# Performance work log

Measured on AMD Instinct MI355X. Metric: run time of the kernel, lower is better.

Reference implementation:

```python
import jax, jax.numpy as jnp
import numpy as np

B, S, D, H = 2, 2048, 2048, 16
DH = D // H


def setup_inputs() -> dict:
    key = jax.random.key(0)
    k1, k2, k3 = jax.random.split(key, 3)
    x = jax.random.normal(k1, (B, S, D), dtype=jnp.float32)
    Wqkv = jax.random.normal(k2, (D, 3 * D), dtype=jnp.float32) * (1.0 / np.sqrt(D))
    bqkv = jnp.zeros((3 * D,), dtype=jnp.float32)
    Wproj = jax.random.normal(k3, (D, D), dtype=jnp.float32) * (1.0 / np.sqrt(D))
    bproj = jnp.zeros((D,), dtype=jnp.float32)
    return {"x": x, "Wqkv": Wqkv, "bqkv": bqkv, "Wproj": Wproj, "bproj": bproj}


def reference(x, Wqkv, bqkv, Wproj, bproj):
    b, s, d = x.shape
    h, dh = H, DH
    # fused qkv projection: [b, s, 3, h, dh]
    qkv = (x @ Wqkv + bqkv).reshape(b, s, 3, h, dh)
    q, k, v = qkv[:, :, 0], qkv[:, :, 1], qkv[:, :, 2]  # each [b, s, h, dh]
    scale = 1.0 / np.sqrt(dh).astype(np.float32)
    # scores [b, h, q, k]
    attn = jnp.einsum('bqhd,bkhd->bhqk', q, k) * scale
    causal = jnp.tril(jnp.ones((s, s), dtype=bool))  # [s, s]
    attn = jnp.where(causal[None, None], attn, -jnp.inf)
    attn = jax.nn.softmax(attn, axis=-1)
    out = jnp.einsum('bhqk,bkhd->bqhd', attn, v).reshape(b, s, d)
    return out @ Wproj + bproj
```

## Files before the change

### kernel.cpp

```cpp
#include <hip/hip_runtime.h>
#include <hip/hip_bf16.h>

#define BB 2
#define SS 2048
#define DD 2048
#define HH 16
#define DHH 128
#define MM 4096
#define NN1 6144
#define NTILES (DD / 64)

typedef __attribute__((ext_vector_type(8))) short bf16x8;
typedef __attribute__((ext_vector_type(4))) float f32x4;
typedef unsigned int u32;

static __device__ __forceinline__ float exp2_hw(float x) {
  return __builtin_amdgcn_exp2f(x);
}

static __device__ __forceinline__ unsigned short f2bf(float f) {
  union { float f; u32 u; } v; v.f = f;
  return (unsigned short)((v.u + 0x7FFFu + ((v.u >> 16) & 1u)) >> 16);
}

static __device__ __forceinline__ void gload_lds16(const void* g, void* l) {
  __builtin_amdgcn_global_load_lds((const __attribute__((address_space(1))) u32*)g,
                                   (__attribute__((address_space(3))) u32*)l, 16, 0, 0);
}

__global__ __launch_bounds__(256) void k_cvt(const float* __restrict__ in,
                                             unsigned short* __restrict__ out) {
  int i = blockIdx.x * 256 + threadIdx.x;
  float4 v = ((const float4*)in)[i];
  ushort4 o;
  o.x = f2bf(v.x); o.y = f2bf(v.y); o.z = f2bf(v.z); o.w = f2bf(v.w);
  ((ushort4*)out)[i] = o;
}

__global__ __launch_bounds__(256) void k_transpose(const float* __restrict__ in,
                                                   unsigned short* __restrict__ out,
                                                   int R, int C) {
  __shared__ float t[32][33];
  int bx = blockIdx.x * 32, by = blockIdx.y * 32;
  int tx = threadIdx.x, ty = threadIdx.y;
  #pragma unroll
  for (int i = ty; i < 32; i += 8)
    t[i][tx] = in[(size_t)(by + i) * C + bx + tx];
  __syncthreads();
  #pragma unroll
  for (int i = ty; i < 32; i += 8)
    out[(size_t)(bx + i) * R + by + tx] = f2bf(t[tx][i]);
}

__device__ __forceinline__ void gemm_core192(const char* __restrict__ Ag,
                                             const char* __restrict__ Bg,
                                             char* lds, f32x4 acc[8][3]) {
  const int tid = threadIdx.x;
  const int wave = tid >> 6, lane = tid & 63;
  const int g = lane >> 4, c = lane & 15;
  const int wm = wave >> 2, wn = wave & 3;

  auto stage = [&](int buf, int kt) {
    char* base = lds + buf * 57344;
    #pragma unroll
    for (int q = 0; q < 4; ++q) {
      int off = q * 8192 + tid * 16;
      int row = off >> 7, cb = off & 127;
      gload_lds16(Ag + (size_t)row * 4096 + kt * 128 + (cb ^ ((row & 7) << 4)),
                  base + q * 8192 + wave * 1024);
    }
    #pragma unroll
    for (int q = 0; q < 3; ++q) {
      int off = q * 8192 + tid * 16;
      int row = off >> 7, cb = off & 127;
      gload_lds16(Bg + (size_t)row * 4096 + kt * 128 + (cb ^ ((row & 7) << 4)),
                  base + 32768 + q * 8192 + wave * 1024);
    }
  };

  stage(0, 0);
  asm volatile("s_waitcnt vmcnt(0)" ::: "memory");
  __builtin_amdgcn_sched_barrier(0);
  __builtin_amdgcn_s_barrier();

  for (int t = 0; t < NTILES; ++t) {
    const char* Ab = lds + (t & 1) * 57344;
    const char* Bb = Ab + 32768;
    bf16x8 af[8][2], bfv[3][2];
    #pragma unroll
    for (int i = 0; i < 8; ++i) {
      int row = wm * 128 + i * 16 + c;
      af[i][0] = *(const bf16x8*)(Ab + row * 128 + ((g * 16) ^ ((row & 7) << 4)));
    }
    #pragma unroll
    for (int j = 0; j < 3; ++j) {
      int row = wn * 48 + j * 16 + c;
      bfv[j][0] = *(const bf16x8*)(Bb + row * 128 + ((g * 16) ^ ((row & 7) << 4)));
    }
    __builtin_amdgcn_sched_barrier(0);
    #pragma unroll
    for (int i = 0; i < 8; ++i) {
      int row = wm * 128 + i * 16 + c;
      af[i][1] = *(const bf16x8*)(Ab + row * 128 + ((64 + g * 16) ^ ((row & 7) << 4)));
    }
    #pragma unroll
    for (int j = 0; j < 3; ++j) {
      int row = wn * 48 + j * 16 + c;
      bfv[j][1] = *(const bf16x8*)(Bb + row * 128 + ((64 + g * 16) ^ ((row & 7) << 4)));
    }
    if (t + 1 < NTILES) stage((t + 1) & 1, t + 1);
    asm volatile("s_waitcnt lgkmcnt(11)" ::: "memory");
    __builtin_amdgcn_sched_barrier(0);
    __builtin_amdgcn_s_setprio(1);
    #pragma unroll
    for (int i = 0; i < 8; ++i)
      #pragma unroll
      for (int j = 0; j < 3; ++j)
        acc[i][j] = __builtin_amdgcn_mfma_f32_16x16x32_bf16(af[i][0], bfv[j][0], acc[i][j], 0, 0, 0);
    __builtin_amdgcn_s_setprio(0);
    asm volatile("s_waitcnt lgkmcnt(0)" ::: "memory");
    __builtin_amdgcn_sched_barrier(0);
    __builtin_amdgcn_s_setprio(1);
    #pragma unroll
    for (int i = 0; i < 8; ++i)
      #pragma unroll
      for (int j = 0; j < 3; ++j)
        acc[i][j] = __builtin_amdgcn_mfma_f32_16x16x32_bf16(af[i][1], bfv[j][1], acc[i][j], 0, 0, 0);
    __builtin_amdgcn_s_setprio(0);
    if (t < NTILES - 1) {
      asm volatile("s_waitcnt vmcnt(0)" ::: "memory");
      __builtin_amdgcn_sched_barrier(0);
      __builtin_amdgcn_s_barrier();
    }
  }
}

__device__ __forceinline__ void gemm_core(const char* __restrict__ Ag,
                                          const char* __restrict__ Bg,
                                          char* Alds, char* Blds,
                                          f32x4 acc[4][4]) {
  const int tid = threadIdx.x;
  const int wave = tid >> 6, lane = tid & 63;
  const int g = lane >> 4, c = lane & 15;
  const int wm = wave >> 1, wn = wave & 1;

  auto stageA = [&](int buf, int kt) {
    #pragma unroll
    for (int q = 0; q < 4; ++q) {
      int off = q * 8192 + wave * 1024 + (lane << 4);
      int row = off >> 7, cb = off & 127;
      gload_lds16(Ag + (size_t)row * 4096 + kt * 128 + (cb ^ ((row & 7) << 4)),
                  Alds + buf * 32768 + q * 8192 + wave * 1024);
    }
  };
  auto stageB = [&](int buf, int kt) {
    #pragma unroll
    for (int q = 0; q < 2; ++q) {
      int off = q * 8192 + wave * 1024 + (lane << 4);
      int row = off >> 7, cb = off & 127;
      gload_lds16(Bg + (size_t)row * 4096 + kt * 128 + (cb ^ ((row & 7) << 4)),
                  Blds + buf * 16384 + q * 8192 + wave * 1024);
    }
  };

  stageA(0, 0); stageB(0, 0);
  stageA(1, 1); stageB(1, 1);
  asm volatile("s_waitcnt vmcnt(6)" ::: "memory");
  __builtin_amdgcn_sched_barrier(0);
  __builtin_amdgcn_s_barrier();

  for (int t = 0; t < NTILES; ++t) {
    const int buf = t % 3;
    const char* Ab = Alds + buf * 32768;
    const char* Bb = Blds + buf * 16384;
    bf16x8 af[4][2], bfv[4][2];
    #pragma unroll
    for (int i = 0; i < 4; ++i) {
      int row = wm * 64 + i * 16 + c;
      af[i][0] = *(const bf16x8*)(Ab + row * 128 + ((g * 16) ^ ((row & 7) << 4)));
    }
    #pragma unroll
    for (int j = 0; j < 4; ++j) {
      int row = wn * 64 + j * 16 + c;
      bfv[j][0] = *(const bf16x8*)(Bb + row * 128 + ((g * 16) ^ ((row & 7) << 4)));
    }
    __builtin_amdgcn_sched_barrier(0);
    #pragma unroll
    for (int i = 0; i < 4; ++i) {
      int row = wm * 64 + i * 16 + c;
      af[i][1] = *(const bf16x8*)(Ab + row * 128 + ((64 + g * 16) ^ ((row & 7) << 4)));
    }
    #pragma unroll
    for (int j = 0; j < 4; ++j) {
      int row = wn * 64 + j * 16 + c;
      bfv[j][1] = *(const bf16x8*)(Bb + row * 128 + ((64 + g * 16) ^ ((row & 7) << 4)));
    }
    if (t + 2 < NTILES) {
      int nb = buf + 2; if (nb >= 3) nb -= 3;
      stageA(nb, t + 2);
      stageB(nb, t + 2);
    }
    asm volatile("s_waitcnt lgkmcnt(8)" ::: "memory");
    __builtin_amdgcn_sched_barrier(0);
    __builtin_amdgcn_s_setprio(1);
    #pragma unroll
    for (int i = 0; i < 4; ++i)
      #pragma unroll
      for (int j = 0; j < 4; ++j)
        acc[i][j] = __builtin_amdgcn_mfma_f32_16x16x32_bf16(af[i][0], bfv[j][0], acc[i][j], 0, 0, 0);
    __builtin_amdgcn_s_setprio(0);
    asm volatile("s_waitcnt lgkmcnt(0)" ::: "memory");
    __builtin_amdgcn_sched_barrier(0);
    __builtin_amdgcn_s_setprio(1);
    #pragma unroll
    for (int i = 0; i < 4; ++i)
      #pragma unroll
      for (int j = 0; j < 4; ++j)
        acc[i][j] = __builtin_amdgcn_mfma_f32_16x16x32_bf16(af[i][1], bfv[j][1], acc[i][j], 0, 0, 0);
    __builtin_amdgcn_s_setprio(0);
    if (t < NTILES - 1) {
      if (t + 2 < NTILES) { asm volatile("s_waitcnt vmcnt(6)" ::: "memory"); }
      else                { asm volatile("s_waitcnt vmcnt(0)" ::: "memory"); }
      __builtin_amdgcn_sched_barrier(0);
      __builtin_amdgcn_s_barrier();
    }
  }
}

__global__ __launch_bounds__(512, 1) void k_gemm1(const unsigned short* __restrict__ A,
                                                  const unsigned short* __restrict__ Bt,
                                                  const float* __restrict__ bias,
                                                  unsigned short* __restrict__ Qb,
                                                  unsigned short* __restrict__ Kb,
                                                  unsigned short* __restrict__ Vt) {
  __shared__ __align__(16) char lds[114688];
  const int x = blockIdx.x & 7, k = blockIdx.x >> 3;
  const int mt = (x & 1) * 8 + (k & 7), nt = (x >> 1) * 8 + (k >> 3);
  const int m0 = mt * 256, n0 = nt * 192;
  f32x4 acc[8][3] = {};
  gemm_core192((const char*)A + (size_t)m0 * 4096,
               (const char*)Bt + (size_t)n0 * 4096,
               lds, acc);
  const int lane = threadIdx.x & 63, wave = threadIdx.x >> 6;
  const int g = lane >> 4, c = lane & 15;
  const int wm = wave >> 2, wn = wave & 3;
  const float qsc = 0.12751879523263566f;
  #pragma unroll
  for (int i = 0; i < 8; ++i) {
    int rowb = m0 + wm * 128 + i * 16 + g * 4;
    int bb = rowb >> 11, s = rowb & 2047;
    #pragma unroll
    for (int j = 0; j < 3; ++j) {
      int gcol = n0 + wn * 48 + j * 16 + c;
      int which = gcol >> 11;
      int head = (gcol >> 7) & 15, dh = gcol & 127;
      float bv = bias[gcol];
      if (which == 2) {
        ushort4 p;
        p.x = f2bf(acc[i][j][0] + bv);
        p.y = f2bf(acc[i][j][1] + bv);
        p.z = f2bf(acc[i][j][2] + bv);
        p.w = f2bf(acc[i][j][3] + bv);
        *(ushort4*)(Vt + ((size_t)(bb * HH + head) * DHH + dh) * SS + s) = p;
      } else {
        float v0 = acc[i][j][0] + bv, v1 = acc[i][j][1] + bv;
        float v2 = acc[i][j][2] + bv, v3 = acc[i][j][3] + bv;
        if (which == 0) { v0 *= qsc; v1 *= qsc; v2 *= qsc; v3 *= qsc; }
        unsigned short* dst = (which == 0 ? Qb : Kb) + ((size_t)(bb * HH + head) * SS + s) * DHH + dh;
        dst[0]       = f2bf(v0);
        dst[DHH]     = f2bf(v1);
        dst[2 * DHH] = f2bf(v2);
        dst[3 * DHH] = f2bf(v3);
      }
    }
  }
}

__global__ __launch_bounds__(512, 1) void k_gemm2(const unsigned short* __restrict__ A,
                                                  const unsigned short* __restrict__ Bt,
                                                  const float* __restrict__ bias,
                                                  float* __restrict__ out) {
  __shared__ __align__(16) char lds[147456];
  const int n0 = blockIdx.x * 128, m0 = blockIdx.y * 256;
  f32x4 acc[4][4] = {};
  gemm_core((const char*)A + (size_t)m0 * 4096,
            (const char*)Bt + (size_t)n0 * 4096,
            lds, lds + 98304, acc);
  const int lane = threadIdx.x & 63, wave = threadIdx.x >> 6;
  const int g = lane >> 4, c = lane & 15;
  const int wm = wave >> 1, wn = wave & 1;
  #pragma unroll
  for (int i = 0; i < 4; ++i) {
    int rowb = m0 + wm * 64 + i * 16 + g * 4;
    #pragma unroll
    for (int j = 0; j < 4; ++j) {
      int gcol = n0 + wn * 64 + j * 16 + c;
      float bv = bias[gcol];
      #pragma unroll
      for (int r = 0; r < 4; ++r)
        out[(size_t)(rowb + r) * DD + gcol] = acc[i][j][r] + bv;
    }
  }
}

__global__ __launch_bounds__(256, 2) void k_attn(const unsigned short* __restrict__ Qb,
                                                 const unsigned short* __restrict__ Kb,
                                                 const unsigned short* __restrict__ Vt,
                                                 unsigned short* __restrict__ O) {
  __shared__ __align__(16) unsigned short Kt[2][64 * 128];
  __shared__ __align__(16) unsigned short Vs[2][128 * 64];
  __shared__ __align__(16) unsigned short Pl[4][32 * 64];
  const int qtl = (blockIdx.y < 16) ? blockIdx.x : (15 - blockIdx.x);
  const int bh = blockIdx.y;
  const int b = bh >> 4, h = bh & 15;
  const int tid = threadIdx.x, wave = tid >> 6, lane = tid & 63;
  const int g = lane >> 4, c = lane & 15;
  const int q0w = qtl * 128 + wave * 32;
  const unsigned short* Qp = Qb + (size_t)bh * SS * DHH;
  const unsigned short* Kp = Kb + (size_t)bh * SS * DHH;
  const unsigned short* Vp = Vt + (size_t)bh * DHH * SS;

  bf16x8 qf[2][4];
  #pragma unroll
  for (int m = 0; m < 2; ++m)
    #pragma unroll
    for (int ks = 0; ks < 4; ++ks)
      qf[m][ks] = *(const bf16x8*)(Qp + (size_t)(q0w + m * 16 + c) * DHH + ks * 32 + g * 8);

  f32x4 acc[2][8] = {};
  float lsum[2] = {0.f, 0.f};

  auto stage = [&](int buf, int kv0) {
    #pragma unroll
    for (int r = 0; r < 4; ++r) {
      int base = r * 4096 + wave * 1024;
      int off = base + (lane << 4);
      { int row = off >> 8; int cb = (off & 255) ^ ((row & 7) << 4);
        gload_lds16((const char*)Kp + (size_t)(kv0 + row) * 256 + cb,
                    (char*)Kt[buf] + base); }
      { int row = off >> 7; int cb = (off & 127) ^ ((row & 7) << 4);
        gload_lds16((const char*)Vp + (size_t)row * (SS * 2) + (size_t)kv0 * 2 + cb,
                    (char*)Vs[buf] + base); }
    }
  };

  const int ntiles = 2 * qtl + 2;
  stage(0, 0);
  __syncthreads();

  for (int t = 0; t < ntiles; ++t) {
    const int cur = t & 1;
    const int kv0 = t * 64;
    if (t + 1 < ntiles) stage(cur ^ 1, kv0 + 64);
    if (kv0 <= q0w + 31) {
      const unsigned short* K_ = Kt[cur];
      const unsigned short* V_ = Vs[cur];
      f32x4 sa[2][4] = {};
      __builtin_amdgcn_s_setprio(1);
      #pragma unroll
      for (int nb = 0; nb < 4; ++nb) {
        const int rk = nb * 16 + c;
        const int swz = (rk & 7) << 4;
        #pragma unroll
        for (int ks = 0; ks < 4; ++ks) {
          bf16x8 kf = *(const bf16x8*)((const char*)K_ + rk * 256 + ((ks * 64 + g * 16) ^ swz));
          sa[0][nb] = __builtin_amdgcn_mfma_f32_16x16x32_bf16(kf, qf[0][ks], sa[0][nb], 0, 0, 0);
          sa[1][nb] = __builtin_amdgcn_mfma_f32_16x16x32_bf16(kf, qf[1][ks], sa[1][nb], 0, 0, 0);
        }
      }
      __builtin_amdgcn_s_setprio(0);
      const bool diag = (kv0 + 63 > q0w);
      #pragma unroll
      for (int m = 0; m < 2; ++m) {
        const int q = q0w + m * 16 + c;
        float p[4][4];
        float rs = 0.f;
        if (diag) {
          #pragma unroll
          for (int nb = 0; nb < 4; ++nb)
            #pragma unroll
            for (int r = 0; r < 4; ++r) {
              float s = (kv0 + nb * 16 + g * 4 + r > q) ? -1e30f : sa[m][nb][r];
              p[nb][r] = exp2_hw(s);
              rs += p[nb][r];
            }
        } else {
          #pragma unroll
          for (int nb = 0; nb < 4; ++nb)
            #pragma unroll
            for (int r = 0; r < 4; ++r) {
              p[nb][r] = exp2_hw(sa[m][nb][r]);
              rs += p[nb][r];
            }
        }
        rs += __shfl_xor(rs, 16, 64);
        rs += __shfl_xor(rs, 32, 64);
        lsum[m] += rs;
        const int rowp = m * 16 + c;
        const int swzp = (rowp & 7) << 4;
        #pragma unroll
        for (int nb = 0; nb < 4; ++nb)
          #pragma unroll
          for (int i2 = 0; i2 < 2; ++i2) {
            u32 w = (u32)f2bf(p[nb][2 * i2]) | ((u32)f2bf(p[nb][2 * i2 + 1]) << 16);
            *(u32*)((char*)Pl[wave] + rowp * 128 + (((nb * 16 + g * 4 + 2 * i2) * 2) ^ swzp)) = w;
          }
      }
      asm volatile("s_waitcnt lgkmcnt(0)" ::: "memory");
      __builtin_amdgcn_sched_barrier(0);
      bf16x8 pf[2][2];
      #pragma unroll
      for (int m = 0; m < 2; ++m)
        #pragma unroll
        for (int c2 = 0; c2 < 2; ++c2) {
          int rowp = m * 16 + c;
          pf[m][c2] = *(const bf16x8*)((const char*)Pl[wave] + rowp * 128 +
                                       ((c2 * 64 + g * 16) ^ ((rowp & 7) << 4)));
        }
      __builtin_amdgcn_s_setprio(1);
      #pragma unroll
      for (int nf = 0; nf < 8; ++nf) {
        const int rv = nf * 16 + c;
        const int swzv = (rv & 7) << 4;
        #pragma unroll
        for (int c2 = 0; c2 < 2; ++c2) {
          bf16x8 vf = *(const bf16x8*)((const char*)V_ + rv * 128 + ((c2 * 64 + g * 16) ^ swzv));
          acc[0][nf] = __builtin_amdgcn_mfma_f32_16x16x32_bf16(pf[0][c2], vf, acc[0][nf], 0, 0, 0);
          acc[1][nf] = __builtin_amdgcn_mfma_f32_16x16x32_bf16(pf[1][c2], vf, acc[1][nf], 0, 0, 0);
        }
      }
      __builtin_amdgcn_s_setprio(0);
    }
    __syncthreads();
  }

  unsigned short* Op = O + (size_t)b * SS * DD + (size_t)h * DHH;
  #pragma unroll
  for (int m = 0; m < 2; ++m) {
    float inv = 1.0f / lsum[m];
    float invr[4];
    #pragma unroll
    for (int r = 0; r < 4; ++r)
      invr[r] = __shfl(inv, 20 * g + r, 64);
    #pragma unroll
    for (int nf = 0; nf < 8; ++nf)
      #pragma unroll
      for (int r = 0; r < 4; ++r) {
        int q = q0w + m * 16 + g * 4 + r;
        Op[(size_t)q * DD + nf * 16 + c] = f2bf(acc[m][nf][r] * invr[r]);
      }
  }
}

extern "C" void kernel_launch(void* const* d_in, const int* in_sizes, int n_in,
                              void* d_out, int out_size, void* d_ws, size_t ws_size,
                              hipStream_t stream) {
  const float* x     = (const float*)d_in[0];
  const float* Wqkv  = (const float*)d_in[1];
  const float* bqkv  = (const float*)d_in[2];
  const float* Wproj = (const float*)d_in[3];
  const float* bproj = (const float*)d_in[4];
  float* out = (float*)d_out;

  char* ws = (char*)d_ws;
  unsigned short* xb  = (unsigned short*)ws; ws += (size_t)MM * DD * 2;
  unsigned short* w1t = (unsigned short*)ws; ws += (size_t)NN1 * DD * 2;
  unsigned short* w2t = (unsigned short*)ws; ws += (size_t)DD * DD * 2;
  unsigned short* Qb  = (unsigned short*)ws; ws += (size_t)BB * HH * SS * DHH * 2;
  unsigned short* Kb  = (unsigned short*)ws; ws += (size_t)BB * HH * SS * DHH * 2;
  unsigned short* Vt  = (unsigned short*)ws; ws += (size_t)BB * HH * SS * DHH * 2;
  unsigned short* Ob  = (unsigned short*)ws; ws += (size_t)MM * DD * 2;

  k_cvt<<<dim3((MM * DD) / 1024), 256, 0, stream>>>(x, xb);
  k_transpose<<<dim3(NN1 / 32, DD / 32), dim3(32, 8), 0, stream>>>(Wqkv, w1t, DD, NN1);
  k_transpose<<<dim3(DD / 32, DD / 32), dim3(32, 8), 0, stream>>>(Wproj, w2t, DD, DD);
  k_gemm1<<<dim3(512), 512, 0, stream>>>(xb, w1t, bqkv, Qb, Kb, Vt);
  k_attn<<<dim3(SS / 128, BB * HH), 256, 0, stream>>>(Qb, Kb, Vt, Ob);
  k_gemm2<<<dim3(DD / 128, MM / 256), 512, 0, stream>>>(Ob, w2t, bproj, out);
}
```

Before: 242.4 us.

## Load K and V fragments directly from global memory in attention, dropping LDS staging

The attention kernel no longer stages K and V tiles into double-buffered shared memory with barriers. Each wave now reads its MFMA fragments for K and V straight from global memory and runs only as many KV tiles as its own causal range needs. Launch bounds go from 2 to 3 blocks per SM, and query tiles are scheduled longest-first. This removes LDS traffic and block-wide synchronisation, but each of the four waves re-reads the same K/V from global/L2, so memory latency is exposed without prefetch.

```diff
diff --git a/kernel.cpp b/kernel.cpp
--- a/kernel.cpp
+++ b/kernel.cpp
@@ -303,14 +303,12 @@
   }
 }
 
-__global__ __launch_bounds__(256, 2) void k_attn(const unsigned short* __restrict__ Qb,
+__global__ __launch_bounds__(256, 3) void k_attn(const unsigned short* __restrict__ Qb,
                                                  const unsigned short* __restrict__ Kb,
                                                  const unsigned short* __restrict__ Vt,
                                                  unsigned short* __restrict__ O) {
-  __shared__ __align__(16) unsigned short Kt[2][64 * 128];
-  __shared__ __align__(16) unsigned short Vs[2][128 * 64];
   __shared__ __align__(16) unsigned short Pl[4][32 * 64];
-  const int qtl = (blockIdx.y < 16) ? blockIdx.x : (15 - blockIdx.x);
+  const int qtl = 15 - blockIdx.x;
   const int bh = blockIdx.y;
   const int b = bh >> 4, h = bh & 15;
   const int tid = threadIdx.x, wave = tid >> 6, lane = tid & 63;
@@ -330,108 +328,82 @@
   f32x4 acc[2][8] = {};
   float lsum[2] = {0.f, 0.f};
 
-  auto stage = [&](int buf, int kv0) {
-    #pragma unroll
-    for (int r = 0; r < 4; ++r) {
-      int base = r * 4096 + wave * 1024;
-      int off = base + (lane << 4);
-      { int row = off >> 8; int cb = (off & 255) ^ ((row & 7) << 4);
-        gload_lds16((const char*)Kp + (size_t)(kv0 + row) * 256 + cb,
-                    (char*)Kt[buf] + base); }
-      { int row = off >> 7; int cb = (off & 127) ^ ((row & 7) << 4);
-        gload_lds16((const char*)Vp + (size_t)row * (SS * 2) + (size_t)kv0 * 2 + cb,
-                    (char*)Vs[buf] + base); }
-    }
-  };
-
-  const int ntiles = 2 * qtl + 2;
-  stage(0, 0);
-  __syncthreads();
-
-  for (int t = 0; t < ntiles; ++t) {
-    const int cur = t & 1;
+  const int ntw = ((q0w + 31) >> 6) + 1;
+  for (int t = 0; t < ntw; ++t) {
     const int kv0 = t * 64;
-    if (t + 1 < ntiles) stage(cur ^ 1, kv0 + 64);
-    if (kv0 <= q0w + 31) {
-      const unsigned short* K_ = Kt[cur];
-      const unsigned short* V_ = Vs[cur];
-      f32x4 sa[2][4] = {};
-      __builtin_amdgcn_s_setprio(1);
-      #pragma unroll
-      for (int nb = 0; nb < 4; ++nb) {
-        const int rk = nb * 16 + c;
-        const int swz = (rk & 7) << 4;
-        #pragma unroll
-        for (int ks = 0; ks < 4; ++ks) {
-          bf16x8 kf = *(const bf16x8*)((const char*)K_ + rk * 256 + ((ks * 64 + g * 16) ^ swz));
-          sa[0][nb] = __builtin_amdgcn_mfma_f32_16x16x32_bf16(kf, qf[0][ks], sa[0][nb], 0, 0, 0);
-          sa[1][nb] = __builtin_amdgcn_mfma_f32_16x16x32_bf16(kf, qf[1][ks], sa[1][nb], 0, 0, 0);
-        }
-      }
-      __builtin_amdgcn_s_setprio(0);
-      const bool diag = (kv0 + 63 > q0w);
-      #pragma unroll
-      for (int m = 0; m < 2; ++m) {
-        const int q = q0w + m * 16 + c;
-        float p[4][4];
-        float rs = 0.f;
-        if (diag) {
-          #pragma unroll
-          for (int nb = 0; nb < 4; ++nb)
-            #pragma unroll
-            for (int r = 0; r < 4; ++r) {
-              float s = (kv0 + nb * 16 + g * 4 + r > q) ? -1e30f : sa[m][nb][r];
-              p[nb][r] = exp2_hw(s);
-              rs += p[nb][r];
-            }
-        } else {
-          #pragma unroll
-          for (int nb = 0; nb < 4; ++nb)
-            #pragma unroll
-            for (int r = 0; r < 4; ++r) {
-              p[nb][r] = exp2_hw(sa[m][nb][r]);
-              rs += p[nb][r];
-            }
-        }
-        rs += __shfl_xor(rs, 16, 64);
-        rs += __shfl_xor(rs, 32, 64);
-        lsum[m] += rs;
-        const int rowp = m * 16 + c;
-        const int swzp = (rowp & 7) << 4;
+    f32x4 sa[2][4] = {};
+    const unsigned short* Kbase = Kp + (size_t)(kv0 + c) * DHH + g * 8;
+    __builtin_amdgcn_s_setprio(1);
+    #pragma unroll
+    for (int nb = 0; nb < 4; ++nb) {
+      #pragma unroll
+      for (int ks = 0; ks < 4; ++ks) {
+        bf16x8 kf = *(const bf16x8*)(Kbase + nb * 16 * DHH + ks * 32);
+        sa[0][nb] = __builtin_amdgcn_mfma_f32_16x16x32_bf16(kf, qf[0][ks], sa[0][nb], 0, 0, 0);
+        sa[1][nb] = __builtin_amdgcn_mfma_f32_16x16x32_bf16(kf, qf[1][ks], sa[1][nb], 0, 0, 0);
+      }
+    }
+    __builtin_amdgcn_s_setprio(0);
+    const bool diag = (kv0 + 63 > q0w);
+    #pragma unroll
+    for (int m = 0; m < 2; ++m) {
+      const int q = q0w + m * 16 + c;
+      float p[4][4];
+      float rs = 0.f;
+      if (diag) {
         #pragma unroll
         for (int nb = 0; nb < 4; ++nb)
           #pragma unroll
-          for (int i2 = 0; i2 < 2; ++i2) {
-            u32 w = (u32)f2bf(p[nb][2 * i2]) | ((u32)f2bf(p[nb][2 * i2 + 1]) << 16);
-            *(u32*)((char*)Pl[wave] + rowp * 128 + (((nb * 16 + g * 4 + 2 * i2) * 2) ^ swzp)) = w;
+          for (int r = 0; r < 4; ++r) {
+            float s = (kv0 + nb * 16 + g * 4 + r > q) ? -1e30f : sa[m][nb][r];
+            p[nb][r] = exp2_hw(s);
+            rs += p[nb][r];
           }
-      }
-      asm volatile("s_waitcnt lgkmcnt(0)" ::: "memory");
-      __builtin_amdgcn_sched_barrier(0);
-      bf16x8 pf[2][2];
-      #pragma unroll
-      for (int m = 0; m < 2; ++m)
+      } else {
         #pragma unroll
-        for (int c2 = 0; c2 < 2; ++c2) {
-          int rowp = m * 16 + c;
-          pf[m][c2] = *(const bf16x8*)((const char*)Pl[wave] + rowp * 128 +
-                                       ((c2 * 64 + g * 16) ^ ((rowp & 7) << 4)));
+        for (int nb = 0; nb < 4; ++nb)
+          #pragma unroll
+          for (int r = 0; r < 4; ++r) {
+            p[nb][r] = exp2_hw(sa[m][nb][r]);
+            rs += p[nb][r];
+          }
+      }
+      rs += __shfl_xor(rs, 16, 64);
+      rs += __shfl_xor(rs, 32, 64);
+      lsum[m] += rs;
+      const int rowp = m * 16 + c;
+      const int swzp = (rowp & 7) << 4;
+      #pragma unroll
+      for (int nb = 0; nb < 4; ++nb)
+        #pragma unroll
+        for (int i2 = 0; i2 < 2; ++i2) {
+          u32 w = (u32)f2bf(p[nb][2 * i2]) | ((u32)f2bf(p[nb][2 * i2 + 1]) << 16);
+          *(u32*)((char*)Pl[wave] + rowp * 128 + (((nb * 16 + g * 4 + 2 * i2) * 2) ^ swzp)) = w;
         }
-      __builtin_amdgcn_s_setprio(1);
-      #pragma unroll
-      for (int nf = 0; nf < 8; ++nf) {
-        const int rv = nf * 16 + c;
-        const int swzv = (rv & 7) << 4;
-        #pragma unroll
-        for (int c2 = 0; c2 < 2; ++c2) {
-          bf16x8 vf = *(const bf16x8*)((const char*)V_ + rv * 128 + ((c2 * 64 + g * 16) ^ swzv));
-          acc[0][nf] = __builtin_amdgcn_mfma_f32_16x16x32_bf16(pf[0][c2], vf, acc[0][nf], 0, 0, 0);
-          acc[1][nf] = __builtin_amdgcn_mfma_f32_16x16x32_bf16(pf[1][c2], vf, acc[1][nf], 0, 0, 0);
-        }
-      }
-      __builtin_amdgcn_s_setprio(0);
-    }
-    __syncthreads();
+    }
+    asm volatile("s_waitcnt lgkmcnt(0)" ::: "memory");
+    __builtin_amdgcn_sched_barrier(0);
+    bf16x8 pf[2][2];
+    #pragma unroll
+    for (int m = 0; m < 2; ++m)
+      #pragma unroll
+      for (int c2 = 0; c2 < 2; ++c2) {
+        int rowp = m * 16 + c;
+        pf[m][c2] = *(const bf16x8*)((const char*)Pl[wave] + rowp * 128 +
+                                     ((c2 * 64 + g * 16) ^ ((rowp & 7) << 4)));
+      }
+    const unsigned short* Vbase = Vp + (size_t)c * SS + kv0 + g * 8;
+    __builtin_amdgcn_s_setprio(1);
+    #pragma unroll
+    for (int nf = 0; nf < 8; ++nf) {
+      #pragma unroll
+      for (int c2 = 0; c2 < 2; ++c2) {
+        bf16x8 vf = *(const bf16x8*)(Vbase + (size_t)nf * 16 * SS + c2 * 32);
+        acc[0][nf] = __builtin_amdgcn_mfma_f32_16x16x32_bf16(pf[0][c2], vf, acc[0][nf], 0, 0, 0);
+        acc[1][nf] = __builtin_amdgcn_mfma_f32_16x16x32_bf16(pf[1][c2], vf, acc[1][nf], 0, 0, 0);
+      }
+    }
+    __builtin_amdgcn_s_setprio(0);
   }
 
   unsigned short* Op = O + (size_t)b * SS * DD + (size_t)h * DHH;
@@ -475,6 +447,6 @@
   k_transpose<<<dim3(NN1 / 32, DD / 32), dim3(32, 8), 0, stream>>>(Wqkv, w1t, DD, NN1);
   k_transpose<<<dim3(DD / 32, DD / 32), dim3(32, 8), 0, stream>>>(Wproj, w2t, DD, DD);
   k_gemm1<<<dim3(512), 512, 0, stream>>>(xb, w1t, bqkv, Qb, Kb, Vt);
-  k_attn<<<dim3(SS / 128, BB * HH), 256, 0, stream>>>(Qb, Kb, Vt, Ob);
+  k_attn<<<dim3(16, BB * HH), 256, 0, stream>>>(Qb, Kb, Vt, Ob);
   k_gemm2<<<dim3(DD / 128, MM / 256), 512, 0, stream>>>(Ob, w2t, bproj, out);
 }
```

Result: slower. 552.1 us (+127.8%).

## Enlarge output-projection GEMM tile to 256x256 with double buffering and swizzled grid

Applied to the files above, without the earlier changes.

The output-projection GEMM moves from 256x128 tiles with a triple-buffered LDS pipeline to 256x256 tiles with a double-buffered pipeline and a 4x2 wave layout. Each wave now computes 128x64, which raises MFMA work per LDS fragment load. A swizzled 1D grid of 128 blocks groups neighbouring tiles for L2 reuse. In exchange, only 128 blocks run on a 256-CU part, and the shallower prefetch with a full vmcnt(0) wait each step may expose global load latency.

```diff
diff --git a/kernel.cpp b/kernel.cpp
--- a/kernel.cpp
+++ b/kernel.cpp
@@ -135,48 +135,44 @@
   }
 }
 
-__device__ __forceinline__ void gemm_core(const char* __restrict__ Ag,
-                                          const char* __restrict__ Bg,
-                                          char* Alds, char* Blds,
-                                          f32x4 acc[4][4]) {
+__device__ __forceinline__ void gemm_core256(const char* __restrict__ Ag,
+                                             const char* __restrict__ Bg,
+                                             char* lds, f32x4 acc[8][4]) {
   const int tid = threadIdx.x;
   const int wave = tid >> 6, lane = tid & 63;
   const int g = lane >> 4, c = lane & 15;
-  const int wm = wave >> 1, wn = wave & 1;
-
-  auto stageA = [&](int buf, int kt) {
+  const int wm = wave >> 2, wn = wave & 3;
+
+  auto stage = [&](int buf, int kt) {
+    char* base = lds + buf * 65536;
     #pragma unroll
     for (int q = 0; q < 4; ++q) {
-      int off = q * 8192 + wave * 1024 + (lane << 4);
+      int off = q * 8192 + tid * 16;
       int row = off >> 7, cb = off & 127;
       gload_lds16(Ag + (size_t)row * 4096 + kt * 128 + (cb ^ ((row & 7) << 4)),
-                  Alds + buf * 32768 + q * 8192 + wave * 1024);
-    }
-  };
-  auto stageB = [&](int buf, int kt) {
-    #pragma unroll
-    for (int q = 0; q < 2; ++q) {
-      int off = q * 8192 + wave * 1024 + (lane << 4);
+                  base + q * 8192 + wave * 1024);
+    }
+    #pragma unroll
+    for (int q = 0; q < 4; ++q) {
+      int off = q * 8192 + tid * 16;
       int row = off >> 7, cb = off & 127;
       gload_lds16(Bg + (size_t)row * 4096 + kt * 128 + (cb ^ ((row & 7) << 4)),
-                  Blds + buf * 16384 + q * 8192 + wave * 1024);
+                  base + 32768 + q * 8192 + wave * 1024);
     }
   };
 
-  stageA(0, 0); stageB(0, 0);
-  stageA(1, 1); stageB(1, 1);
-  asm volatile("s_waitcnt vmcnt(6)" ::: "memory");
+  stage(0, 0);
+  asm volatile("s_waitcnt vmcnt(0)" ::: "memory");
   __builtin_amdgcn_sched_barrier(0);
   __builtin_amdgcn_s_barrier();
 
   for (int t = 0; t < NTILES; ++t) {
-    const int buf = t % 3;
-    const char* Ab = Alds + buf * 32768;
-    const char* Bb = Blds + buf * 16384;
-    bf16x8 af[4][2], bfv[4][2];
-    #pragma unroll
-    for (int i = 0; i < 4; ++i) {
-      int row = wm * 64 + i * 16 + c;
+    const char* Ab = lds + (t & 1) * 65536;
+    const char* Bb = Ab + 32768;
+    bf16x8 af[8][2], bfv[4][2];
+    #pragma unroll
+    for (int i = 0; i < 8; ++i) {
+      int row = wm * 128 + i * 16 + c;
       af[i][0] = *(const bf16x8*)(Ab + row * 128 + ((g * 16) ^ ((row & 7) << 4)));
     }
     #pragma unroll
@@ -186,8 +182,8 @@
     }
     __builtin_amdgcn_sched_barrier(0);
     #pragma unroll
-    for (int i = 0; i < 4; ++i) {
-      int row = wm * 64 + i * 16 + c;
+    for (int i = 0; i < 8; ++i) {
+      int row = wm * 128 + i * 16 + c;
       af[i][1] = *(const bf16x8*)(Ab + row * 128 + ((64 + g * 16) ^ ((row & 7) << 4)));
     }
     #pragma unroll
@@ -195,16 +191,12 @@
       int row = wn * 64 + j * 16 + c;
       bfv[j][1] = *(const bf16x8*)(Bb + row * 128 + ((64 + g * 16) ^ ((row & 7) << 4)));
     }
-    if (t + 2 < NTILES) {
-      int nb = buf + 2; if (nb >= 3) nb -= 3;
-      stageA(nb, t + 2);
-      stageB(nb, t + 2);
-    }
-    asm volatile("s_waitcnt lgkmcnt(8)" ::: "memory");
+    if (t + 1 < NTILES) stage((t + 1) & 1, t + 1);
+    asm volatile("s_waitcnt lgkmcnt(12)" ::: "memory");
     __builtin_amdgcn_sched_barrier(0);
     __builtin_amdgcn_s_setprio(1);
     #pragma unroll
-    for (int i = 0; i < 4; ++i)
+    for (int i = 0; i < 8; ++i)
       #pragma unroll
       for (int j = 0; j < 4; ++j)
         acc[i][j] = __builtin_amdgcn_mfma_f32_16x16x32_bf16(af[i][0], bfv[j][0], acc[i][j], 0, 0, 0);
@@ -213,14 +205,13 @@
     __builtin_amdgcn_sched_barrier(0);
     __builtin_amdgcn_s_setprio(1);
     #pragma unroll
-    for (int i = 0; i < 4; ++i)
+    for (int i = 0; i < 8; ++i)
       #pragma unroll
       for (int j = 0; j < 4; ++j)
         acc[i][j] = __builtin_amdgcn_mfma_f32_16x16x32_bf16(af[i][1], bfv[j][1], acc[i][j], 0, 0, 0);
     __builtin_amdgcn_s_setprio(0);
     if (t < NTILES - 1) {
-      if (t + 2 < NTILES) { asm volatile("s_waitcnt vmcnt(6)" ::: "memory"); }
-      else                { asm volatile("s_waitcnt vmcnt(0)" ::: "memory"); }
+      asm volatile("s_waitcnt vmcnt(0)" ::: "memory");
       __builtin_amdgcn_sched_barrier(0);
       __builtin_amdgcn_s_barrier();
     }
@@ -280,18 +271,20 @@
                                                   const unsigned short* __restrict__ Bt,
                                                   const float* __restrict__ bias,
                                                   float* __restrict__ out) {
-  __shared__ __align__(16) char lds[147456];
-  const int n0 = blockIdx.x * 128, m0 = blockIdx.y * 256;
-  f32x4 acc[4][4] = {};
-  gemm_core((const char*)A + (size_t)m0 * 4096,
-            (const char*)Bt + (size_t)n0 * 4096,
-            lds, lds + 98304, acc);
+  __shared__ __align__(16) char lds[131072];
+  const int x = blockIdx.x & 7, k = blockIdx.x >> 3;
+  const int mt = (x & 3) * 4 + (k & 3), nt = (x >> 2) * 4 + (k >> 2);
+  const int m0 = mt * 256, n0 = nt * 256;
+  f32x4 acc[8][4] = {};
+  gemm_core256((const char*)A + (size_t)m0 * 4096,
+               (const char*)Bt + (size_t)n0 * 4096,
+               lds, acc);
   const int lane = threadIdx.x & 63, wave = threadIdx.x >> 6;
   const int g = lane >> 4, c = lane & 15;
-  const int wm = wave >> 1, wn = wave & 1;
-  #pragma unroll
-  for (int i = 0; i < 4; ++i) {
-    int rowb = m0 + wm * 64 + i * 16 + g * 4;
+  const int wm = wave >> 2, wn = wave & 3;
+  #pragma unroll
+  for (int i = 0; i < 8; ++i) {
+    int rowb = m0 + wm * 128 + i * 16 + g * 4;
     #pragma unroll
     for (int j = 0; j < 4; ++j) {
       int gcol = n0 + wn * 64 + j * 16 + c;
@@ -475,6 +468,6 @@
   k_transpose<<<dim3(NN1 / 32, DD / 32), dim3(32, 8), 0, stream>>>(Wqkv, w1t, DD, NN1);
   k_transpose<<<dim3(DD / 32, DD / 32), dim3(32, 8), 0, stream>>>(Wproj, w2t, DD, DD);
   k_gemm1<<<dim3(512), 512, 0, stream>>>(xb, w1t, bqkv, Qb, Kb, Vt);
-  k_attn<<<dim3(SS / 128, BB * HH), 256, 0, stream>>>(Qb, Kb, Vt, Ob);
-  k_gemm2<<<dim3(DD / 128, MM / 256), 512, 0, stream>>>(Ob, w2t, bproj, out);
-}
+  k_attn<<<dim3(16, BB * HH), 256, 0, stream>>>(Qb, Kb, Vt, Ob);
+  k_gemm2<<<dim3(128), 512, 0, stream>>>(Ob, w2t, bproj, out);
+}
```

After: 256.4 us. 1.06x slower.
